# Optimization experiments

Hardware: AMD Instinct MI355X
Metric: run time of the kernel (lower is better)

The kernel has to match this reference:

```python
import jax, jax.numpy as jnp
import numpy as np

H = 256  # hidden size (hardcoded in module)
F_IN = 10  # input features (hardcoded via x.view(..., 10))


def _lstm_cell(x, h, c, w_ih, w_hh, b_ih, b_hh):
    # PyTorch gate order: i, f, g, o. gates: [B, 4H]
    gates = x @ w_ih.T + h @ w_hh.T + b_ih + b_hh
    i, f, g, o = jnp.split(gates, 4, axis=-1)
    c_new = jax.nn.sigmoid(f) * c + jax.nn.sigmoid(i) * jnp.tanh(g)
    h_new = jax.nn.sigmoid(o) * jnp.tanh(c_new)
    return h_new, c_new


def setup_inputs() -> dict:
    key = jax.random.key(0)
    ks = jax.random.split(key, 13)
    B, T = 512, 1024
    s = 0.05
    return {
        "x": jax.random.normal(ks[0], (B, T, F_IN), dtype=jnp.float32),
        "w_ih0": jax.random.normal(ks[1], (4 * H, F_IN), dtype=jnp.float32) * s,
        "w_hh0": jax.random.normal(ks[2], (4 * H, H), dtype=jnp.float32) * s,
        "b_ih0": jax.random.normal(ks[3], (4 * H,), dtype=jnp.float32) * s,
        "b_hh0": jax.random.normal(ks[4], (4 * H,), dtype=jnp.float32) * s,
        "w_ih1": jax.random.normal(ks[5], (4 * H, H), dtype=jnp.float32) * s,
        "w_hh1": jax.random.normal(ks[6], (4 * H, H), dtype=jnp.float32) * s,
        "b_ih1": jax.random.normal(ks[7], (4 * H,), dtype=jnp.float32) * s,
        "b_hh1": jax.random.normal(ks[8], (4 * H,), dtype=jnp.float32) * s,
        "adv_w1": jax.random.normal(ks[9], (H, H), dtype=jnp.float32) * s,
        "adv_b1": jax.random.normal(ks[10], (H,), dtype=jnp.float32) * s,
        "adv_w2": jax.random.normal(ks[11], (1, H), dtype=jnp.float32) * s,
        "adv_b2": jax.random.normal(ks[12], (1,), dtype=jnp.float32) * s,
    }


def reference(x, w_ih0, w_hh0, b_ih0, b_hh0, w_ih1, w_hh1, b_ih1, b_hh1,
              adv_w1, adv_b1, adv_w2, adv_b2):
    B, T, _ = x.shape
    h0 = jnp.zeros((B, H), dtype=x.dtype)

    def step(carry, x_t):
        h1, c1, h2, c2 = carry
        h1, c1 = _lstm_cell(x_t, h1, c1, w_ih0, w_hh0, b_ih0, b_hh0)
        h2, c2 = _lstm_cell(h1, h2, c2, w_ih1, w_hh1, b_ih1, b_hh1)
        return (h1, c1, h2, c2), h2

    xs = jnp.swapaxes(x, 0, 1)  # [T, B, F_IN]
    _, hs = jax.lax.scan(step, (h0, h0, h0, h0), xs)  # hs: [T, B, H]

    # advantage MLP head applied per-timestep
    hidden = jax.nn.relu(jnp.einsum('tbh,oh->tbo', hs, adv_w1) + adv_b1)
    scores = jnp.einsum('tbh,oh->tbo', hidden, adv_w2) + adv_b2  # [T, B, 1]

    # Faithful to torch.cat(outputs).view(B, -1): flatten TIME-major, then
    # reinterpret as [B, T] (mixes batch and time when B != T).
    flat = scores.reshape(-1)            # time-major flat buffer [T*B]
    mixed = flat.reshape(B, T)
    advantage = jax.nn.softmax(mixed, axis=1)
    return advantage.reshape(-1)
```

## Files before the change

### kernel.cpp

```cpp
#include <hip/hip_runtime.h>
#include <cstdint>
#include <cstddef>

#define Tn 1024
#define Bn 512
#define Hn 256

#define H1S 264
#define H2S 264
#define WHS 264
#define GWS 20

#define H1_OFF  0
#define H2_OFF  (H1_OFF + 16*H1S*2)
#define XB_OFF  (H2_OFF + 16*H2S*2)
#define WH_OFF  (XB_OFF + 2*16*16*2)
#define GW_OFF  (WH_OFF + 16*WHS*2)
#define B1_OFF  (GW_OFF + 4*16*GWS*4)
#define B2_OFF  (B1_OFF + 64*4)
#define BH_OFF  (B2_OFF + 64*4)
#define W2H_OFF (BH_OFF + 16*4)
#define DEAD_OFF (W2H_OFF + 16*4)
#define LDS_TOTAL 79872

#define SCORES_OFF 0
#define H1G_OFF  (2*1024*1024)
#define H2G_OFF  (3*1024*1024)
#define FLAG_OFF (4*1024*1024)
#define WS_USED  (4*1024*1024 + 8192)

#define POLL_GUARD (1 << 22)

typedef _Float16 v4h __attribute__((ext_vector_type(4)));
typedef float    v4f __attribute__((ext_vector_type(4)));
typedef unsigned int u32x4 __attribute__((ext_vector_type(4)));
typedef unsigned long long u64;

__device__ inline float sigm(float x){ return 1.0f/(1.0f + __expf(-x)); }
__device__ inline float tanh_f(float x){ return 1.0f - 2.0f/(1.0f + __expf(2.0f*x)); }

__device__ inline v4h cvt4(float4 a){
    v4h f; f[0]=(_Float16)a.x; f[1]=(_Float16)a.y; f[2]=(_Float16)a.z; f[3]=(_Float16)a.w;
    return f;
}

__device__ inline bool poll32(const int* tags, int tgt){
    int idx = threadIdx.x & 31;
    int guard = 0;
    while (true){
        int t = __hip_atomic_load(&tags[idx], __ATOMIC_RELAXED, __HIP_MEMORY_SCOPE_AGENT);
        if (__ballot(t < tgt) == 0ull) return true;
        if (++guard > POLL_GUARD) return false;
        __builtin_amdgcn_s_sleep(1);
    }
}

#define LADDR(oo) ( (size_t)(((oo)>>9)*528 + ((oo)&511)) )
__device__ __forceinline__ void stage_tile8(const char* gbase, char* lbase, int t){
    u32x4 q0,q1,q2,q3;
    const char* p0 = gbase + t*16;
    const char* p1 = p0 + 2048;
    const char* p2 = p0 + 4096;
    const char* p3 = p0 + 6144;
    asm volatile("global_load_dwordx4 %0, %1, off sc0 sc1" : "=v"(q0) : "v"(p0));
    asm volatile("global_load_dwordx4 %0, %1, off sc0 sc1" : "=v"(q1) : "v"(p1));
    asm volatile("global_load_dwordx4 %0, %1, off sc0 sc1" : "=v"(q2) : "v"(p2));
    asm volatile("global_load_dwordx4 %0, %1, off sc0 sc1" : "=v"(q3) : "v"(p3));
    asm volatile("s_waitcnt vmcnt(0)"
                 : "+v"(q0), "+v"(q1), "+v"(q2), "+v"(q3) :: "memory");
    const int o = t*16;
    *(u32x4*)(lbase + LADDR(o))        = q0;
    *(u32x4*)(lbase + LADDR(o + 2048)) = q1;
    *(u32x4*)(lbase + LADDR(o + 4096)) = q2;
    *(u32x4*)(lbase + LADDR(o + 6144)) = q3;
}

__device__ __forceinline__ void lstm_ew_publish(v4f acc, float* gw, const float* bs,
                                                int n, float& c, _Float16* dst,
                                                int ln15, int ln4)
{
    #pragma unroll
    for (int r = 0; r < 4; ++r) gw[(ln4*4 + r)*GWS + ln15] = acc[r];
    asm volatile("s_waitcnt lgkmcnt(0)" ::: "memory");
    v4f g4 = *(const v4f*)(gw + ln15*GWS + ln4*4);
    asm volatile("s_waitcnt lgkmcnt(0)" ::: "memory");
    v4f bb = *(const v4f*)(bs + n*16 + ln4*4);
    float gi = sigm(g4.x + bb.x), gf = sigm(g4.y + bb.y);
    float gg = tanh_f(g4.z + bb.z), go = sigm(g4.w + bb.w);
    c = gf*c + gi*gg;
    float hn = go * tanh_f(c);
    union { _Float16 h; unsigned short u; } cvt; cvt.h = (_Float16)hn;
    unsigned v32 = cvt.u;
    unsigned p16 = (unsigned)__shfl_xor((int)v32, 16, 64);
    unsigned lo32 = v32 | (p16 << 16);
    unsigned hi32 = (unsigned)__shfl_xor((int)lo32, 32, 64);
    if (ln4 == 0){
        u64 pk = (u64)lo32 | ((u64)hi32 << 32);
        __hip_atomic_store((u64*)dst, pk, __ATOMIC_RELAXED, __HIP_MEMORY_SCOPE_AGENT);
    }
}

__global__ __launch_bounds__(256)
void lstm_pipe(const float* __restrict__ x,
               const float* __restrict__ w_ih0, const float* __restrict__ w_hh0,
               const float* __restrict__ b_ih0, const float* __restrict__ b_hh0,
               const float* __restrict__ w_ih1, const float* __restrict__ w_hh1,
               const float* __restrict__ b_ih1, const float* __restrict__ b_hh1,
               const float* __restrict__ adv_w1, const float* __restrict__ adv_b1,
               const float* __restrict__ adv_w2,
               float* __restrict__ scores, _Float16* __restrict__ h1g,
               _Float16* __restrict__ h2g, int* __restrict__ flags)
{
    extern __shared__ char smem[];
    _Float16* H1l = (_Float16*)(smem + H1_OFF);
    _Float16* H2l = (_Float16*)(smem + H2_OFF);
    _Float16* XBp = (_Float16*)(smem + XB_OFF);
    _Float16* WHl = (_Float16*)(smem + WH_OFF);
    float* gatesc = (float*)(smem + GW_OFF);
    float* b1s    = (float*)(smem + B1_OFF);
    float* b2s    = (float*)(smem + B2_OFF);
    float* bhs    = (float*)(smem + BH_OFF);
    float* w2hs   = (float*)(smem + W2H_OFF);
    volatile int* deadp = (volatile int*)(smem + DEAD_OFF);

    const int tid  = threadIdx.x;
    const int lane = tid & 63;
    const int wv   = tid >> 6;
    const int ln15 = lane & 15;
    const int ln4  = lane >> 4;
    const int rt = blockIdx.x >> 4;
    const int us = blockIdx.x & 15;
    const int r0 = rt * 16;
    const int u0 = us * 16;
    const int eng = wv >> 1;
    const int wq  = wv & 1;
    const int n0  = wq * 2;

    int* tags1 = flags;
    int* tags2 = flags + 1024;

    if (tid == 0) *deadp = 0;

    const int N0i = n0*16 + ln15;
    const int R0 = (N0i & 3)*256 + u0 + (N0i >> 2);
    const int N1i = N0i + 16;
    const int R1 = (N1i & 3)*256 + u0 + (N1i >> 2);
    v4h W[64];
    if (eng == 0){
        #pragma unroll
        for (int t = 0; t < 2; ++t){
            const int R = t ? R1 : R0;
            v4h f;
            #pragma unroll
            for (int j = 0; j < 4; ++j){
                int c = ln4*4 + j;
                f[j] = (_Float16)((c < 10) ? w_ih0[R*10 + c] : 0.f);
            }
            W[t] = f;
        }
        #pragma unroll
        for (int k = 0; k < 16; ++k){
            float4 a0 = *(const float4*)(w_hh0 + (size_t)R0*256 + k*16 + ln4*4);
            float4 a1 = *(const float4*)(w_hh0 + (size_t)R1*256 + k*16 + ln4*4);
            W[2+k]  = cvt4(a0);
            W[18+k] = cvt4(a1);
        }
    } else {
        #pragma unroll
        for (int k = 0; k < 16; ++k){
            float4 a0 = *(const float4*)(w_ih1 + (size_t)R0*256 + k*16 + ln4*4);
            float4 a1 = *(const float4*)(w_ih1 + (size_t)R1*256 + k*16 + ln4*4);
            float4 b0 = *(const float4*)(w_hh1 + (size_t)R0*256 + k*16 + ln4*4);
            float4 b1 = *(const float4*)(w_hh1 + (size_t)R1*256 + k*16 + ln4*4);
            W[k]    = cvt4(a0);
            W[16+k] = cvt4(a1);
            W[32+k] = cvt4(b0);
            W[48+k] = cvt4(b1);
        }
    }

    for (int idx = tid; idx < 16*WHS; idx += 256){
        int n = idx / WHS, c = idx - n*WHS;
        float v = (c < 256) ? adv_w1[(u0+n)*256 + c] : 0.f;
        WHl[idx] = (_Float16)v;
    }
    if (tid < 64){
        int R = (tid & 3)*256 + u0 + (tid >> 2);
        b1s[tid] = b_ih0[R] + b_hh0[R];
        b2s[tid] = b_ih1[R] + b_hh1[R];
    }
    if (tid < 16){
        bhs[tid]  = adv_b1[u0 + tid];
        w2hs[tid] = adv_w2[u0 + tid];
    }
    for (int idx = tid; idx < 512; idx += 256) XBp[idx] = (_Float16)0.f;
    __syncthreads();
    if (tid < 16){
        const float* xp = x + ((size_t)(r0 + tid)*Tn + 0)*10;
        #pragma unroll
        for (int i = 0; i < 10; ++i) XBp[tid*16 + i] = (_Float16)xp[i];
    }
    __syncthreads();

    float ca = 0.f, cb = 0.f;
    float* gw = gatesc + wv*(16*GWS);

    for (int tau = 0; tau <= Tn + 1; ++tau){
        float xr[10];
        if (wv == 3 && lane < 16 && tau + 1 < Tn){
            const float* xp = x + ((size_t)(r0 + lane)*Tn + (tau+1))*10;
            #pragma unroll
            for (int i = 0; i < 10; ++i) xr[i] = xp[i];
        }
        if (wv == 0 && tau >= 1 && tau <= Tn){
            if (!poll32(tags1 + rt*32, tau) && lane == 0) *deadp = 1;
        }
        if (wv == 2 && tau >= 2){
            if (!poll32(tags2 + rt*32, tau - 1) && lane == 0) *deadp = 1;
        }
        asm volatile("" ::: "memory");
        __syncthreads();
        if (*deadp) return;

        if (eng == 0){
            if (tau <= Tn){
                const int slot = (tau + 3) & 3;
                stage_tile8((const char*)(h1g + (size_t)slot*(Bn*Hn) + (size_t)r0*Hn),
                            (char*)H1l, tid);
            }
        } else {
            if (tau >= 1){
                const int slot = (tau + 2) & 3;
                stage_tile8((const char*)(h2g + (size_t)slot*(Bn*Hn) + (size_t)r0*Hn),
                            (char*)H2l, tid - 128);
            }
        }
        __syncthreads();

        if (eng == 0){
            if (tau < Tn){
                v4f acc0 = {0.f,0.f,0.f,0.f}, acc1 = {0.f,0.f,0.f,0.f};
                {
                    v4h a = *(const v4h*)(XBp + (tau & 1)*256 + ln15*16 + ln4*4);
                    acc0 = __builtin_amdgcn_mfma_f32_16x16x16f16(a, W[0], acc0, 0,0,0);
                    acc1 = __builtin_amdgcn_mfma_f32_16x16x16f16(a, W[1], acc1, 0,0,0);
                }
                const _Float16* Ap = H1l + ln15*H1S + ln4*4;
                #pragma unroll
                for (int k = 0; k < 16; ++k){
                    v4h a = *(const v4h*)(Ap + k*16);
                    acc0 = __builtin_amdgcn_mfma_f32_16x16x16f16(a, W[2+k],  acc0, 0,0,0);
                    acc1 = __builtin_amdgcn_mfma_f32_16x16x16f16(a, W[18+k], acc1, 0,0,0);
                }
                _Float16* d0 = h1g + (size_t)(tau & 3)*(Bn*Hn)
                             + (size_t)(r0 + ln15)*Hn + u0 + n0*4;
                lstm_ew_publish(acc0, gw, b1s, n0,   ca, d0,     ln15, ln4);
                lstm_ew_publish(acc1, gw, b1s, n0+1, cb, d0 + 4, ln15, ln4);
                asm volatile("s_waitcnt vmcnt(0)" ::: "memory");
                if (lane == 0)
                    __hip_atomic_store(&tags1[rt*32 + us*2 + wq], tau + 1,
                                       __ATOMIC_RELAXED, __HIP_MEMORY_SCOPE_AGENT);
            }
        } else {
            if (wv == 3 && lane < 16 && tau + 1 < Tn){
                _Float16* xd = XBp + ((tau+1) & 1)*256 + lane*16;
                #pragma unroll
                for (int i = 0; i < 10; ++i) xd[i] = (_Float16)xr[i];
            }
            if (tau >= 1 && tau <= Tn){
                v4f acc0 = {0.f,0.f,0.f,0.f}, acc1 = {0.f,0.f,0.f,0.f};
                const _Float16* Ap1 = H1l + ln15*H1S + ln4*4;
                const _Float16* Ap2 = H2l + ln15*H2S + ln4*4;
                #pragma unroll
                for (int k = 0; k < 16; ++k){
                    v4h a = *(const v4h*)(Ap1 + k*16);
                    acc0 = __builtin_amdgcn_mfma_f32_16x16x16f16(a, W[k],    acc0, 0,0,0);
                    acc1 = __builtin_amdgcn_mfma_f32_16x16x16f16(a, W[16+k], acc1, 0,0,0);
                }
                #pragma unroll
                for (int k = 0; k < 16; ++k){
                    v4h a = *(const v4h*)(Ap2 + k*16);
                    acc0 = __builtin_amdgcn_mfma_f32_16x16x16f16(a, W[32+k], acc0, 0,0,0);
                    acc1 = __builtin_amdgcn_mfma_f32_16x16x16f16(a, W[48+k], acc1, 0,0,0);
                }
                _Float16* d0 = h2g + (size_t)((tau + 3) & 3)*(Bn*Hn)
                             + (size_t)(r0 + ln15)*Hn + u0 + n0*4;
                lstm_ew_publish(acc0, gw, b2s, n0,   ca, d0,     ln15, ln4);
                lstm_ew_publish(acc1, gw, b2s, n0+1, cb, d0 + 4, ln15, ln4);
                asm volatile("s_waitcnt vmcnt(0)" ::: "memory");
                if (lane == 0)
                    __hip_atomic_store(&tags2[rt*32 + us*2 + wq], tau,
                                       __ATOMIC_RELAXED, __HIP_MEMORY_SCOPE_AGENT);
            }
            if (wv == 2 && tau >= 2){
                v4f acc = {0.f,0.f,0.f,0.f};
                const _Float16* Ap = H2l + ln15*H2S + ln4*4;
                const _Float16* Bp = WHl + ln15*WHS + ln4*4;
                #pragma unroll
                for (int k = 0; k < 16; ++k)
                    acc = __builtin_amdgcn_mfma_f32_16x16x16f16(*(const v4h*)(Ap + k*16),
                                                                *(const v4h*)(Bp + k*16), acc, 0, 0, 0);
                float bh = bhs[ln15], w2 = w2hs[ln15];
                float t0 = fmaxf(acc[0] + bh, 0.f) * w2;
                float t1 = fmaxf(acc[1] + bh, 0.f) * w2;
                float t2 = fmaxf(acc[2] + bh, 0.f) * w2;
                float t3 = fmaxf(acc[3] + bh, 0.f) * w2;
                #pragma unroll
                for (int mk = 1; mk <= 8; mk <<= 1){
                    t0 += __shfl_xor(t0, mk, 64);
                    t1 += __shfl_xor(t1, mk, 64);
                    t2 += __shfl_xor(t2, mk, 64);
                    t3 += __shfl_xor(t3, mk, 64);
                }
                if (ln15 == 0){
                    float* sp = scores + (size_t)(tau - 2)*Bn + r0 + ln4*4;
                    atomicAdd(sp + 0, t0);
                    atomicAdd(sp + 1, t1);
                    atomicAdd(sp + 2, t2);
                    atomicAdd(sp + 3, t3);
                }
            }
        }
        __syncthreads();
    }
}

__global__ __launch_bounds__(256)
void softmax_adv(const float* __restrict__ scores, float* __restrict__ out)
{
    const int b = blockIdx.x, tid = threadIdx.x;
    const int lane = tid & 63, wv = tid >> 6;
    __shared__ float red[4];
    const float4* sp = (const float4*)(scores + (size_t)b*1024);
    float4 v = sp[tid];
    float m = fmaxf(fmaxf(v.x, v.y), fmaxf(v.z, v.w));
    #pragma unroll
    for (int o = 32; o > 0; o >>= 1) m = fmaxf(m, __shfl_xor(m, o, 64));
    if (lane == 0) red[wv] = m;
    __syncthreads();
    m = fmaxf(fmaxf(red[0], red[1]), fmaxf(red[2], red[3]));
    __syncthreads();
    float e0 = __expf(v.x - m), e1 = __expf(v.y - m);
    float e2 = __expf(v.z - m), e3 = __expf(v.w - m);
    float s = e0 + e1 + e2 + e3;
    #pragma unroll
    for (int o = 32; o > 0; o >>= 1) s += __shfl_xor(s, o, 64);
    if (lane == 0) red[wv] = s;
    __syncthreads();
    s = red[0] + red[1] + red[2] + red[3];
    float inv = 1.0f / s;
    float4 o4; o4.x = e0*inv; o4.y = e1*inv; o4.z = e2*inv; o4.w = e3*inv;
    ((float4*)(out + (size_t)b*1024))[tid] = o4;
}

extern "C" void kernel_launch(void* const* d_in, const int* in_sizes, int n_in,
                              void* d_out, int out_size, void* d_ws, size_t ws_size,
                              hipStream_t stream)
{
    (void)in_sizes; (void)n_in; (void)out_size; (void)ws_size;
    const float* x      = (const float*)d_in[0];
    const float* w_ih0  = (const float*)d_in[1];
    const float* w_hh0  = (const float*)d_in[2];
    const float* b_ih0  = (const float*)d_in[3];
    const float* b_hh0  = (const float*)d_in[4];
    const float* w_ih1  = (const float*)d_in[5];
    const float* w_hh1  = (const float*)d_in[6];
    const float* b_ih1  = (const float*)d_in[7];
    const float* b_hh1  = (const float*)d_in[8];
    const float* adv_w1 = (const float*)d_in[9];
    const float* adv_b1 = (const float*)d_in[10];
    const float* adv_w2 = (const float*)d_in[11];

    float*    scores = (float*)((char*)d_ws + SCORES_OFF);
    _Float16* h1g    = (_Float16*)((char*)d_ws + H1G_OFF);
    _Float16* h2g    = (_Float16*)((char*)d_ws + H2G_OFF);
    int*      flags  = (int*)((char*)d_ws + FLAG_OFF);

    hipMemsetAsync(d_ws, 0, WS_USED, stream);
    hipFuncSetAttribute((const void*)lstm_pipe,
                        hipFuncAttributeMaxDynamicSharedMemorySize, LDS_TOTAL);

    hipLaunchKernelGGL(lstm_pipe, dim3(512), dim3(256), LDS_TOTAL, stream,
                       x, w_ih0, w_hh0, b_ih0, b_hh0, w_ih1, w_hh1, b_ih1, b_hh1,
                       adv_w1, adv_b1, adv_w2, scores, h1g, h2g, flags);
    hipLaunchKernelGGL(softmax_adv, dim3(512), dim3(256), 0, stream,
                       scores, (float*)d_out);
}
```

Measured before the change: 3.924 ms.

## Decouple layer-0 and layer-1 wave pairs with LDS barriers and separate h1 buffers

Replaces the block-wide __syncthreads lockstep with per-engine LDS counter barriers, so the layer-0 waves and the layer-1 waves each run their own time loop. Layer 0 can run up to two steps ahead, bounded by an LDS progress counter. Layer 1 gets its own staged copy of h1, and each wave pair stages its whole tile with eight loads per lane. The intent is to stop one layer's global polling and staging from stalling the other layer. The cost is spin-waiting on LDS counters and the added risk of deadlock or ordering bugs.

```diff
diff --git a/kernel.cpp b/kernel.cpp
--- a/kernel.cpp
+++ b/kernel.cpp
@@ -11,16 +11,17 @@
 #define WHS 264
 #define GWS 20
 
-#define H1_OFF  0
-#define H2_OFF  (H1_OFF + 16*H1S*2)
-#define XB_OFF  (H2_OFF + 16*H2S*2)
-#define WH_OFF  (XB_OFF + 2*16*16*2)
-#define GW_OFF  (WH_OFF + 16*WHS*2)
-#define B1_OFF  (GW_OFF + 4*16*GWS*4)
-#define B2_OFF  (B1_OFF + 64*4)
-#define BH_OFF  (B2_OFF + 64*4)
-#define W2H_OFF (BH_OFF + 16*4)
-#define DEAD_OFF (W2H_OFF + 16*4)
+#define H1_OFF   0
+#define H1B_OFF  (H1_OFF + 16*H1S*2)
+#define H2_OFF   (H1B_OFF + 16*H1S*2)
+#define XB_OFF   (H2_OFF + 16*H2S*2)
+#define WH_OFF   (XB_OFF + 2*16*16*2)
+#define GW_OFF   (WH_OFF + 16*WHS*2)
+#define B1_OFF   (GW_OFF + 4*16*GWS*4)
+#define B2_OFF   (B1_OFF + 64*4)
+#define BH_OFF   (B2_OFF + 64*4)
+#define W2H_OFF  (BH_OFF + 16*4)
+#define SYNC_OFF (W2H_OFF + 16*4)
 #define LDS_TOTAL 79872
 
 #define SCORES_OFF 0
@@ -55,24 +56,42 @@
     }
 }
 
+__device__ __forceinline__ bool ebar2(volatile int* c, int target, volatile int* deadp){
+    asm volatile("s_waitcnt lgkmcnt(0)" ::: "memory");
+    if ((threadIdx.x & 63) == 0) atomicAdd((int*)c, 1);
+    int guard = 0;
+    while (*c < target){
+        if (*deadp) return false;
+        if (++guard > POLL_GUARD){ *deadp = 1; return false; }
+    }
+    asm volatile("" ::: "memory");
+    return true;
+}
+
 #define LADDR(oo) ( (size_t)(((oo)>>9)*528 + ((oo)&511)) )
-__device__ __forceinline__ void stage_tile8(const char* gbase, char* lbase, int t){
-    u32x4 q0,q1,q2,q3;
-    const char* p0 = gbase + t*16;
-    const char* p1 = p0 + 2048;
-    const char* p2 = p0 + 4096;
-    const char* p3 = p0 + 6144;
-    asm volatile("global_load_dwordx4 %0, %1, off sc0 sc1" : "=v"(q0) : "v"(p0));
-    asm volatile("global_load_dwordx4 %0, %1, off sc0 sc1" : "=v"(q1) : "v"(p1));
-    asm volatile("global_load_dwordx4 %0, %1, off sc0 sc1" : "=v"(q2) : "v"(p2));
-    asm volatile("global_load_dwordx4 %0, %1, off sc0 sc1" : "=v"(q3) : "v"(p3));
+__device__ __forceinline__ void stage_tile8w(const char* gbase, char* lbase, int l){
+    u32x4 q0,q1,q2,q3,q4,q5,q6,q7;
+    const char* p = gbase + l*16;
+    asm volatile("global_load_dwordx4 %0, %1, off sc0 sc1" : "=v"(q0) : "v"(p));
+    asm volatile("global_load_dwordx4 %0, %1, off sc0 sc1" : "=v"(q1) : "v"(p+1024));
+    asm volatile("global_load_dwordx4 %0, %1, off sc0 sc1" : "=v"(q2) : "v"(p+2048));
+    asm volatile("global_load_dwordx4 %0, %1, off sc0 sc1" : "=v"(q3) : "v"(p+3072));
+    asm volatile("global_load_dwordx4 %0, %1, off sc0 sc1" : "=v"(q4) : "v"(p+4096));
+    asm volatile("global_load_dwordx4 %0, %1, off sc0 sc1" : "=v"(q5) : "v"(p+5120));
+    asm volatile("global_load_dwordx4 %0, %1, off sc0 sc1" : "=v"(q6) : "v"(p+6144));
+    asm volatile("global_load_dwordx4 %0, %1, off sc0 sc1" : "=v"(q7) : "v"(p+7168));
     asm volatile("s_waitcnt vmcnt(0)"
-                 : "+v"(q0), "+v"(q1), "+v"(q2), "+v"(q3) :: "memory");
-    const int o = t*16;
+                 : "+v"(q0), "+v"(q1), "+v"(q2), "+v"(q3),
+                   "+v"(q4), "+v"(q5), "+v"(q6), "+v"(q7) :: "memory");
+    const int o = l*16;
     *(u32x4*)(lbase + LADDR(o))        = q0;
-    *(u32x4*)(lbase + LADDR(o + 2048)) = q1;
-    *(u32x4*)(lbase + LADDR(o + 4096)) = q2;
-    *(u32x4*)(lbase + LADDR(o + 6144)) = q3;
+    *(u32x4*)(lbase + LADDR(o + 1024)) = q1;
+    *(u32x4*)(lbase + LADDR(o + 2048)) = q2;
+    *(u32x4*)(lbase + LADDR(o + 3072)) = q3;
+    *(u32x4*)(lbase + LADDR(o + 4096)) = q4;
+    *(u32x4*)(lbase + LADDR(o + 5120)) = q5;
+    *(u32x4*)(lbase + LADDR(o + 6144)) = q6;
+    *(u32x4*)(lbase + LADDR(o + 7168)) = q7;
 }
 
 __device__ __forceinline__ void lstm_ew_publish(v4f acc, float* gw, const float* bs,
@@ -113,6 +132,7 @@
 {
     extern __shared__ char smem[];
     _Float16* H1l = (_Float16*)(smem + H1_OFF);
+    _Float16* H1B = (_Float16*)(smem + H1B_OFF);
     _Float16* H2l = (_Float16*)(smem + H2_OFF);
     _Float16* XBp = (_Float16*)(smem + XB_OFF);
     _Float16* WHl = (_Float16*)(smem + WH_OFF);
@@ -121,7 +141,10 @@
     float* b2s    = (float*)(smem + B2_OFF);
     float* bhs    = (float*)(smem + BH_OFF);
     float* w2hs   = (float*)(smem + W2H_OFF);
-    volatile int* deadp = (volatile int*)(smem + DEAD_OFF);
+    volatile int* eb0   = (volatile int*)(smem + SYNC_OFF);
+    volatile int* eb1   = (volatile int*)(smem + SYNC_OFF + 4);
+    volatile int* e1p   = (volatile int*)(smem + SYNC_OFF + 8);
+    volatile int* deadp = (volatile int*)(smem + SYNC_OFF + 12);
 
     const int tid  = threadIdx.x;
     const int lane = tid & 63;
@@ -139,7 +162,7 @@
     int* tags1 = flags;
     int* tags2 = flags + 1024;
 
-    if (tid == 0) *deadp = 0;
+    if (tid == 0){ *eb0 = 0; *eb1 = 0; *e1p = 0; *deadp = 0; }
 
     const int N0i = n0*16 + ln15;
     const int R0 = (N0i & 3)*256 + u0 + (N0i >> 2);
@@ -205,71 +228,88 @@
     float ca = 0.f, cb = 0.f;
     float* gw = gatesc + wv*(16*GWS);
 
-    for (int tau = 0; tau <= Tn + 1; ++tau){
-        float xr[10];
-        if (wv == 3 && lane < 16 && tau + 1 < Tn){
-            const float* xp = x + ((size_t)(r0 + lane)*Tn + (tau+1))*10;
+    if (eng == 0){
+        int bgen = 0;
+        for (int tau = 0; tau < Tn; ++tau){
+            float xr[10];
+            if (wq == 1 && lane < 16 && tau + 1 < Tn){
+                const float* xp = x + ((size_t)(r0 + lane)*Tn + (tau+1))*10;
+                #pragma unroll
+                for (int i = 0; i < 10; ++i) xr[i] = xp[i];
+            }
+            if (tau >= 3){
+                int guard = 0;
+                while (*e1p < tau - 2){
+                    if (*deadp) return;
+                    if (++guard > POLL_GUARD){ *deadp = 1; return; }
+                }
+            }
+            if (wq == 0){
+                if (tau >= 1){
+                    if (!poll32(tags1 + rt*32, tau)){ *deadp = 1; return; }
+                }
+                asm volatile("" ::: "memory");
+                const int slot = (tau + 3) & 3;
+                stage_tile8w((const char*)(h1g + (size_t)slot*(Bn*Hn) + (size_t)r0*Hn),
+                             (char*)H1l, lane);
+            } else {
+                if (lane < 16 && tau + 1 < Tn){
+                    _Float16* xd = XBp + ((tau+1) & 1)*256 + lane*16;
+                    #pragma unroll
+                    for (int i = 0; i < 10; ++i) xd[i] = (_Float16)xr[i];
+                }
+            }
+            ++bgen; if (!ebar2(eb0, 2*bgen, deadp)) return;
+
+            v4f acc0 = {0.f,0.f,0.f,0.f}, acc1 = {0.f,0.f,0.f,0.f};
+            {
+                v4h a = *(const v4h*)(XBp + (tau & 1)*256 + ln15*16 + ln4*4);
+                acc0 = __builtin_amdgcn_mfma_f32_16x16x16f16(a, W[0], acc0, 0,0,0);
+                acc1 = __builtin_amdgcn_mfma_f32_16x16x16f16(a, W[1], acc1, 0,0,0);
+            }
+            const _Float16* Ap = H1l + ln15*H1S + ln4*4;
             #pragma unroll
-            for (int i = 0; i < 10; ++i) xr[i] = xp[i];
+            for (int k = 0; k < 16; ++k){
+                v4h a = *(const v4h*)(Ap + k*16);
+                acc0 = __builtin_amdgcn_mfma_f32_16x16x16f16(a, W[2+k],  acc0, 0,0,0);
+                acc1 = __builtin_amdgcn_mfma_f32_16x16x16f16(a, W[18+k], acc1, 0,0,0);
+            }
+            _Float16* d0 = h1g + (size_t)(tau & 3)*(Bn*Hn)
+                         + (size_t)(r0 + ln15)*Hn + u0 + n0*4;
+            lstm_ew_publish(acc0, gw, b1s, n0,   ca, d0,     ln15, ln4);
+            lstm_ew_publish(acc1, gw, b1s, n0+1, cb, d0 + 4, ln15, ln4);
+            asm volatile("s_waitcnt vmcnt(0)" ::: "memory");
+            if (lane == 0)
+                __hip_atomic_store(&tags1[rt*32 + us*2 + wq], tau + 1,
+                                   __ATOMIC_RELAXED, __HIP_MEMORY_SCOPE_AGENT);
+            ++bgen; if (!ebar2(eb0, 2*bgen, deadp)) return;
         }
-        if (wv == 0 && tau >= 1 && tau <= Tn){
-            if (!poll32(tags1 + rt*32, tau) && lane == 0) *deadp = 1;
-        }
-        if (wv == 2 && tau >= 2){
-            if (!poll32(tags2 + rt*32, tau - 1) && lane == 0) *deadp = 1;
-        }
-        asm volatile("" ::: "memory");
-        __syncthreads();
-        if (*deadp) return;
-
-        if (eng == 0){
+    } else {
+        int bgen = 0;
+        for (int tau = 1; tau <= Tn + 1; ++tau){
+            if (wq == 0){
+                if (tau <= Tn){
+                    if (!poll32(tags1 + rt*32, tau)){ *deadp = 1; return; }
+                    asm volatile("" ::: "memory");
+                    const int slot = (tau + 3) & 3;
+                    stage_tile8w((const char*)(h1g + (size_t)slot*(Bn*Hn) + (size_t)r0*Hn),
+                                 (char*)H1B, lane);
+                }
+            } else {
+                if (tau >= 2){
+                    if (!poll32(tags2 + rt*32, tau - 1)){ *deadp = 1; return; }
+                }
+                asm volatile("" ::: "memory");
+                const int slot = (tau + 2) & 3;
+                stage_tile8w((const char*)(h2g + (size_t)slot*(Bn*Hn) + (size_t)r0*Hn),
+                             (char*)H2l, lane);
+            }
+            ++bgen; if (!ebar2(eb1, 2*bgen, deadp)) return;
+            if (wq == 0 && lane == 0) *e1p = tau;
+
             if (tau <= Tn){
-                const int slot = (tau + 3) & 3;
-                stage_tile8((const char*)(h1g + (size_t)slot*(Bn*Hn) + (size_t)r0*Hn),
-                            (char*)H1l, tid);
-            }
-        } else {
-            if (tau >= 1){
-                const int slot = (tau + 2) & 3;
-                stage_tile8((const char*)(h2g + (size_t)slot*(Bn*Hn) + (size_t)r0*Hn),
-                            (char*)H2l, tid - 128);
-            }
-        }
-        __syncthreads();
-
-        if (eng == 0){
-            if (tau < Tn){
                 v4f acc0 = {0.f,0.f,0.f,0.f}, acc1 = {0.f,0.f,0.f,0.f};
-                {
-                    v4h a = *(const v4h*)(XBp + (tau & 1)*256 + ln15*16 + ln4*4);
-                    acc0 = __builtin_amdgcn_mfma_f32_16x16x16f16(a, W[0], acc0, 0,0,0);
-                    acc1 = __builtin_amdgcn_mfma_f32_16x16x16f16(a, W[1], acc1, 0,0,0);
-                }
-                const _Float16* Ap = H1l + ln15*H1S + ln4*4;
-                #pragma unroll
-                for (int k = 0; k < 16; ++k){
-                    v4h a = *(const v4h*)(Ap + k*16);
-                    acc0 = __builtin_amdgcn_mfma_f32_16x16x16f16(a, W[2+k],  acc0, 0,0,0);
-                    acc1 = __builtin_amdgcn_mfma_f32_16x16x16f16(a, W[18+k], acc1, 0,0,0);
-                }
-                _Float16* d0 = h1g + (size_t)(tau & 3)*(Bn*Hn)
-                             + (size_t)(r0 + ln15)*Hn + u0 + n0*4;
-                lstm_ew_publish(acc0, gw, b1s, n0,   ca, d0,     ln15, ln4);
-                lstm_ew_publish(acc1, gw, b1s, n0+1, cb, d0 + 4, ln15, ln4);
-                asm volatile("s_waitcnt vmcnt(0)" ::: "memory");
-                if (lane == 0)
-                    __hip_atomic_store(&tags1[rt*32 + us*2 + wq], tau + 1,
-                                       __ATOMIC_RELAXED, __HIP_MEMORY_SCOPE_AGENT);
-            }
-        } else {
-            if (wv == 3 && lane < 16 && tau + 1 < Tn){
-                _Float16* xd = XBp + ((tau+1) & 1)*256 + lane*16;
-                #pragma unroll
-                for (int i = 0; i < 10; ++i) xd[i] = (_Float16)xr[i];
-            }
-            if (tau >= 1 && tau <= Tn){
-                v4f acc0 = {0.f,0.f,0.f,0.f}, acc1 = {0.f,0.f,0.f,0.f};
-                const _Float16* Ap1 = H1l + ln15*H1S + ln4*4;
+                const _Float16* Ap1 = H1B + ln15*H1S + ln4*4;
                 const _Float16* Ap2 = H2l + ln15*H2S + ln4*4;
                 #pragma unroll
                 for (int k = 0; k < 16; ++k){
@@ -292,7 +332,7 @@
                     __hip_atomic_store(&tags2[rt*32 + us*2 + wq], tau,
                                        __ATOMIC_RELAXED, __HIP_MEMORY_SCOPE_AGENT);
             }
-            if (wv == 2 && tau >= 2){
+            if (wq == 0 && tau >= 2){
                 v4f acc = {0.f,0.f,0.f,0.f};
                 const _Float16* Ap = H2l + ln15*H2S + ln4*4;
                 const _Float16* Bp = WHl + ln15*WHS + ln4*4;
@@ -320,8 +360,8 @@
                     atomicAdd(sp + 3, t3);
                 }
             }
+            ++bgen; if (!ebar2(eb1, 2*bgen, deadp)) return;
         }
-        __syncthreads();
     }
 }
 
```

New measurement: 4.691 ms. 19.5% more time.
